# Kernel optimization log

Hardware: AMD Instinct MI355X
Metric: run time of the kernel (lower is better)

The kernel has to match this reference:

```python
import jax, jax.numpy as jnp
import numpy as np

H, B, T, DH = 16, 2, 2048, 64
MODEL_DIM = 1024


def setup_inputs() -> dict:
    key = jax.random.key(0)
    ks = jax.random.split(key, 5)
    q = jax.random.normal(ks[0], (H, B, T, DH), dtype=jnp.float32)
    k = jax.random.normal(ks[1], (H, B, T, DH), dtype=jnp.float32)
    v = jax.random.normal(ks[2], (H, B, T, DH), dtype=jnp.float32)
    Wo_w = jax.random.normal(ks[3], (MODEL_DIM, H * DH), dtype=jnp.float32) * 0.02
    Wo_b = jax.random.normal(ks[4], (MODEL_DIM,), dtype=jnp.float32) * 0.02
    return {"q": q, "k": k, "v": v, "Wo_w": Wo_w, "Wo_b": Wo_b}


def reference(q, k, v, Wo_w, Wo_b):
    # per-head scaled dot-product attention; scale uses per-head dk (=DH)
    scale = jnp.sqrt(jnp.asarray(DH, dtype=q.dtype))
    # scores: [H, B, T, T]
    scores = jnp.einsum('hbtd,hbsd->hbts', q, k) / scale
    # causal mask (additive -1e12 on strict upper triangle, matching torch code)
    mask = jnp.triu(jnp.ones((T, T), dtype=bool), 1)
    scores = scores + (-1e12) * mask.astype(scores.dtype)
    weights = jax.nn.softmax(scores, axis=-1)
    # context per head: [H, B, T, DH]
    context = jnp.einsum('hbts,hbsd->hbtd', weights, v)
    # concat heads along feature dim: [B, T, H*DH]
    context = jnp.transpose(context, (1, 2, 0, 3)).reshape(B, T, H * DH)
    # output projection (torch Linear: x @ W.T + b)
    return context @ Wo_w.T + Wo_b
```

## Files before the change

kernel.cpp:

```cpp
#include <hip/hip_runtime.h>

typedef __attribute__((ext_vector_type(8))) short bf16x8;
typedef __attribute__((ext_vector_type(4))) float f32x4;
typedef __attribute__((ext_vector_type(4))) unsigned int u32x4;
typedef __attribute__((ext_vector_type(4))) unsigned short u16x4;

#define H_ 16
#define B_ 2
#define T_ 2048
#define DH_ 64
#define MD_ 1024

static __device__ inline unsigned short f2bf(float f) {
    union { float f; unsigned u; } x; x.f = f;
    unsigned r = (x.u + 0x7fffu + ((x.u >> 16) & 1u)) >> 16;
    return (unsigned short)r;
}
static __device__ inline unsigned int pack_bf2(float lo, float hi) {
    return __builtin_amdgcn_perm(__float_as_uint(hi), __float_as_uint(lo), 0x07060302u);
}
static __device__ inline unsigned short hi16(float f) {
    return (unsigned short)(__float_as_uint(f) >> 16);
}

__global__ void cvt_k(const float* __restrict__ w, unsigned short* __restrict__ o, int n) {
    int i = (blockIdx.x * blockDim.x + threadIdx.x) * 4;
    if (i < n) {
        f32x4 x = *(const f32x4*)(w + i);
        u16x4 y;
        y[0] = f2bf(x[0]); y[1] = f2bf(x[1]); y[2] = f2bf(x[2]); y[3] = f2bf(x[3]);
        *(u16x4*)(o + i) = y;
    }
}

__global__ __launch_bounds__(256) void attn_k(const float* __restrict__ q,
                                              const float* __restrict__ k,
                                              const float* __restrict__ v,
                                              unsigned short* __restrict__ ctx) {
    const int flat = blockIdx.x;
    const int xcd = flat & 7, idx = flat >> 3;
    const int hb = xcd * 4 + (idx & 3);
    const int pair = idx >> 2;
    const int h = hb >> 1, b = hb & 1;
    const int tid = threadIdx.x;
    const int wave = tid >> 6, lane = tid & 63;
    const int ln = lane & 15, quad = lane >> 4;

    __shared__ __attribute__((aligned(16))) unsigned short kt[64][72];
    __shared__ __attribute__((aligned(16))) unsigned short vt[64][72];
    __shared__ __attribute__((aligned(16))) unsigned short pl[4][16][72];

    const long base = (long)hb * (T_ * DH_);
    const int krow = tid >> 2, kc = (tid & 3) * 16;
    const int vkp = tid & 31, vdg = tid >> 5;

    bf16x8 ones;
#pragma unroll
    for (int i = 0; i < 8; i++) ones[i] = (short)0x3F80;

#pragma unroll 1
    for (int halfsel = 0; halfsel < 2; halfsel++) {
        const int t = halfsel ? (31 - pair) : pair;
        const int nsteps = t + 1;
        const int q0w = t * 64 + wave * 16;

        bf16x8 qf0, qf1;
        {
            const float* qp = q + base + (long)(q0w + ln) * DH_ + quad * 8;
            f32x4 a0 = *(const f32x4*)qp;
            f32x4 a1 = *(const f32x4*)(qp + 4);
            f32x4 b0 = *(const f32x4*)(qp + 32);
            f32x4 b1 = *(const f32x4*)(qp + 36);
#pragma unroll
            for (int j = 0; j < 4; j++) {
                qf0[j]   = (short)f2bf(a0[j] * 0.125f);
                qf0[4+j] = (short)f2bf(a1[j] * 0.125f);
                qf1[j]   = (short)f2bf(b0[j] * 0.125f);
                qf1[4+j] = (short)f2bf(b1[j] * 0.125f);
            }
        }

        f32x4 oacc[4];
#pragma unroll
        for (int i = 0; i < 4; i++) oacc[i] = f32x4{0.f, 0.f, 0.f, 0.f};
        f32x4 lacc = f32x4{0.f, 0.f, 0.f, 0.f};

        f32x4 kr[4], va[2], vb[2];
        {
            const float* kp_ = k + base + (long)krow * DH_ + kc;
#pragma unroll
            for (int i = 0; i < 4; i++) kr[i] = *(const f32x4*)(kp_ + i * 4);
            const float* vp_ = v + base + (long)(2 * vkp) * DH_ + vdg * 8;
            va[0] = *(const f32x4*)vp_;       va[1] = *(const f32x4*)(vp_ + 4);
            vb[0] = *(const f32x4*)(vp_ + DH_); vb[1] = *(const f32x4*)(vp_ + DH_ + 4);
        }

#pragma unroll 1
        for (int step = 0; step < nsteps; step++) {
            __syncthreads();
            {
                u32x4 w0, w1;
                w0[0] = pack_bf2(kr[0][0], kr[0][1]); w0[1] = pack_bf2(kr[0][2], kr[0][3]);
                w0[2] = pack_bf2(kr[1][0], kr[1][1]); w0[3] = pack_bf2(kr[1][2], kr[1][3]);
                w1[0] = pack_bf2(kr[2][0], kr[2][1]); w1[1] = pack_bf2(kr[2][2], kr[2][3]);
                w1[2] = pack_bf2(kr[3][0], kr[3][1]); w1[3] = pack_bf2(kr[3][2], kr[3][3]);
                *(u32x4*)&kt[krow][kc]     = w0;
                *(u32x4*)&kt[krow][kc + 8] = w1;
#pragma unroll
                for (int j = 0; j < 4; j++)
                    ((unsigned int*)&vt[vdg * 8 + j][0])[vkp]     = pack_bf2(va[0][j], vb[0][j]);
#pragma unroll
                for (int j = 0; j < 4; j++)
                    ((unsigned int*)&vt[vdg * 8 + 4 + j][0])[vkp] = pack_bf2(va[1][j], vb[1][j]);
            }
            __syncthreads();

            if (step + 1 < nsteps) {
                const float* kp_ = k + base + (long)((step + 1) * 64 + krow) * DH_ + kc;
#pragma unroll
                for (int i = 0; i < 4; i++) kr[i] = *(const f32x4*)(kp_ + i * 4);
                const float* vp_ = v + base + (long)((step + 1) * 64 + 2 * vkp) * DH_ + vdg * 8;
                va[0] = *(const f32x4*)vp_;         va[1] = *(const f32x4*)(vp_ + 4);
                vb[0] = *(const f32x4*)(vp_ + DH_); vb[1] = *(const f32x4*)(vp_ + DH_ + 4);
            }

            f32x4 sa[4];
#pragma unroll
            for (int nt = 0; nt < 4; nt++) {
                bf16x8 kf0 = *(const bf16x8*)&kt[nt * 16 + ln][quad * 8];
                bf16x8 kf1 = *(const bf16x8*)&kt[nt * 16 + ln][32 + quad * 8];
                f32x4 a = f32x4{0.f, 0.f, 0.f, 0.f};
                a = __builtin_amdgcn_mfma_f32_16x16x32_bf16(qf0, kf0, a, 0, 0, 0);
                a = __builtin_amdgcn_mfma_f32_16x16x32_bf16(qf1, kf1, a, 0, 0, 0);
                sa[nt] = a;
            }

            if (step == nsteps - 1) {
                const int lr = wave * 16 + quad * 4;
#pragma unroll
                for (int nt = 0; nt < 4; nt++)
#pragma unroll
                    for (int r = 0; r < 4; r++) {
                        float p = __expf(sa[nt][r]);
                        if (nt * 16 + ln > lr + r) p = 0.f;
                        pl[wave][quad * 4 + r][nt * 16 + ln] = hi16(p);
                    }
            } else {
#pragma unroll
                for (int nt = 0; nt < 4; nt++)
#pragma unroll
                    for (int r = 0; r < 4; r++)
                        pl[wave][quad * 4 + r][nt * 16 + ln] = hi16(__expf(sa[nt][r]));
            }

            bf16x8 pf0 = *(const bf16x8*)&pl[wave][ln][quad * 8];
            bf16x8 pf1 = *(const bf16x8*)&pl[wave][ln][32 + quad * 8];

            lacc = __builtin_amdgcn_mfma_f32_16x16x32_bf16(pf0, ones, lacc, 0, 0, 0);
            lacc = __builtin_amdgcn_mfma_f32_16x16x32_bf16(pf1, ones, lacc, 0, 0, 0);

#pragma unroll
            for (int dt = 0; dt < 4; dt++) {
                bf16x8 vf0 = *(const bf16x8*)&vt[dt * 16 + ln][quad * 8];
                bf16x8 vf1 = *(const bf16x8*)&vt[dt * 16 + ln][32 + quad * 8];
                oacc[dt] = __builtin_amdgcn_mfma_f32_16x16x32_bf16(pf0, vf0, oacc[dt], 0, 0, 0);
                oacc[dt] = __builtin_amdgcn_mfma_f32_16x16x32_bf16(pf1, vf1, oacc[dt], 0, 0, 0);
            }
        }

#pragma unroll
        for (int r = 0; r < 4; r++) {
            float rl = __builtin_amdgcn_rcpf(lacc[r]);
            int row_g = q0w + quad * 4 + r;
#pragma unroll
            for (int dt = 0; dt < 4; dt++)
                ctx[(long)(b * T_ + row_g) * MD_ + h * 64 + dt * 16 + ln] =
                    f2bf(oacc[dt][r] * rl);
        }
    }
}

__global__ __launch_bounds__(256) void proj_k(const unsigned short* __restrict__ A,
                                              const unsigned short* __restrict__ Bw,
                                              const float* __restrict__ bias,
                                              float* __restrict__ out) {
    const int flat = blockIdx.x;
    const int xcd = flat & 7, idx = flat >> 3;
    const int n0 = (xcd * 2 + (idx & 1)) * 64;
    const int m0 = (idx >> 1) * 128;
    const int tid = threadIdx.x;
    const int wave = tid >> 6, lane = tid & 63;
    const int wm = wave >> 1, wn = wave & 1;
    const int ln = lane & 15, quad = lane >> 4;

    __shared__ __attribute__((aligned(16))) unsigned short As[128][72];
    __shared__ __attribute__((aligned(16))) unsigned short Bs[64][72];

    const int arow = tid >> 1, ac = (tid & 1) * 32;
    const int brow = tid >> 2, bc = (tid & 3) * 16;

    f32x4 acc[4][2];
#pragma unroll
    for (int i = 0; i < 4; i++)
#pragma unroll
        for (int j = 0; j < 2; j++) acc[i][j] = f32x4{0.f, 0.f, 0.f, 0.f};

    u32x4 ar[4], br[2];
    {
        const unsigned short* ap = A + (long)(m0 + arow) * 1024 + ac;
#pragma unroll
        for (int i = 0; i < 4; i++) ar[i] = *(const u32x4*)(ap + i * 8);
        const unsigned short* bp = Bw + (long)(n0 + brow) * 1024 + bc;
        br[0] = *(const u32x4*)bp; br[1] = *(const u32x4*)(bp + 8);
    }

#pragma unroll 1
    for (int ks = 0; ks < 1024; ks += 64) {
        __syncthreads();
#pragma unroll
        for (int i = 0; i < 4; i++) *(u32x4*)&As[arow][ac + i * 8] = ar[i];
        *(u32x4*)&Bs[brow][bc] = br[0];
        *(u32x4*)&Bs[brow][bc + 8] = br[1];
        __syncthreads();

        if (ks + 64 < 1024) {
            const unsigned short* ap = A + (long)(m0 + arow) * 1024 + ks + 64 + ac;
#pragma unroll
            for (int i = 0; i < 4; i++) ar[i] = *(const u32x4*)(ap + i * 8);
            const unsigned short* bp = Bw + (long)(n0 + brow) * 1024 + ks + 64 + bc;
            br[0] = *(const u32x4*)bp; br[1] = *(const u32x4*)(bp + 8);
        }

        bf16x8 af[4][2], bfr[2][2];
#pragma unroll
        for (int mt = 0; mt < 4; mt++) {
            af[mt][0] = *(const bf16x8*)&As[wm * 64 + mt * 16 + ln][quad * 8];
            af[mt][1] = *(const bf16x8*)&As[wm * 64 + mt * 16 + ln][32 + quad * 8];
        }
#pragma unroll
        for (int nt = 0; nt < 2; nt++) {
            bfr[nt][0] = *(const bf16x8*)&Bs[wn * 32 + nt * 16 + ln][quad * 8];
            bfr[nt][1] = *(const bf16x8*)&Bs[wn * 32 + nt * 16 + ln][32 + quad * 8];
        }
#pragma unroll
        for (int mt = 0; mt < 4; mt++)
#pragma unroll
            for (int nt = 0; nt < 2; nt++) {
                acc[mt][nt] = __builtin_amdgcn_mfma_f32_16x16x32_bf16(af[mt][0], bfr[nt][0], acc[mt][nt], 0, 0, 0);
                acc[mt][nt] = __builtin_amdgcn_mfma_f32_16x16x32_bf16(af[mt][1], bfr[nt][1], acc[mt][nt], 0, 0, 0);
            }
    }

#pragma unroll
    for (int nt = 0; nt < 2; nt++) {
        int col = n0 + wn * 32 + nt * 16 + ln;
        float bz = bias[col];
#pragma unroll
        for (int mt = 0; mt < 4; mt++)
#pragma unroll
            for (int r = 0; r < 4; r++) {
                int row = m0 + wm * 64 + mt * 16 + quad * 4 + r;
                out[(long)row * 1024 + col] = acc[mt][nt][r] + bz;
            }
    }
}

extern "C" void kernel_launch(void* const* d_in, const int* in_sizes, int n_in,
                              void* d_out, int out_size, void* d_ws, size_t ws_size,
                              hipStream_t stream) {
    const float* q    = (const float*)d_in[0];
    const float* k    = (const float*)d_in[1];
    const float* v    = (const float*)d_in[2];
    const float* Wo_w = (const float*)d_in[3];
    const float* Wo_b = (const float*)d_in[4];
    float* out = (float*)d_out;

    unsigned short* ctx = (unsigned short*)d_ws;
    unsigned short* wob = ctx + (size_t)4096 * 1024;

    cvt_k<<<1024, 256, 0, stream>>>(Wo_w, wob, MD_ * MD_);
    attn_k<<<512, 256, 0, stream>>>(q, k, v, ctx);
    proj_k<<<512, 256, 0, stream>>>(ctx, wob, Wo_b, out);
}
```

Measured before the change: 159.5 us.

## Pre-convert K and transposed V to bf16, split attention and projection grids

A new prep kernel converts K to bf16 and V to a transposed bf16 layout once, alongside the weight conversion. The attention kernel can then copy K and V tiles straight into LDS without packing or strided writes. Previously every query tile re-converted the same K and V from fp32. The attention grid now runs one query tile per block with 1024 blocks instead of pairing two tiles per block. The projection kernel uses 64x64 tiles, doubling its block count for more parallelism. In exchange it adds an extra global write and read of K and V and an extra prep pass.

Measured after the change: 153.5 us. 3.7% less time.

```diff
diff --git a/kernel.cpp b/kernel.cpp
--- a/kernel.cpp
+++ b/kernel.cpp
@@ -23,24 +23,71 @@
     return (unsigned short)(__float_as_uint(f) >> 16);
 }
 
-__global__ void cvt_k(const float* __restrict__ w, unsigned short* __restrict__ o, int n) {
-    int i = (blockIdx.x * blockDim.x + threadIdx.x) * 4;
-    if (i < n) {
+__global__ __launch_bounds__(256) void prep_k(const float* __restrict__ k,
+                                              const float* __restrict__ v,
+                                              const float* __restrict__ w,
+                                              unsigned short* __restrict__ kb,
+                                              unsigned short* __restrict__ vtb,
+                                              unsigned short* __restrict__ wob) {
+    __shared__ __attribute__((aligned(16))) unsigned short vt64[64][64];
+    const int blk = blockIdx.x;
+    const int tid = threadIdx.x;
+    if (blk < 1024) {
+        int i = (blk * 256 + tid) * 4;
         f32x4 x = *(const f32x4*)(w + i);
         u16x4 y;
         y[0] = f2bf(x[0]); y[1] = f2bf(x[1]); y[2] = f2bf(x[2]); y[3] = f2bf(x[3]);
-        *(u16x4*)(o + i) = y;
-    }
-}
-
-__global__ __launch_bounds__(256) void attn_k(const float* __restrict__ q,
-                                              const float* __restrict__ k,
-                                              const float* __restrict__ v,
-                                              unsigned short* __restrict__ ctx) {
-    const int flat = blockIdx.x;
-    const int xcd = flat & 7, idx = flat >> 3;
-    const int hb = xcd * 4 + (idx & 3);
-    const int pair = idx >> 2;
+        *(u16x4*)(wob + i) = y;
+    } else if (blk < 2048) {
+        int j = blk - 1024;
+        const int hb = j >> 5, s0 = (j & 31) * 64;
+        const int row = tid >> 2, c = (tid & 3) * 16;
+        const long off = (long)hb * (T_ * DH_) + (long)(s0 + row) * DH_ + c;
+        const float* p = k + off;
+        f32x4 a0 = *(const f32x4*)p;
+        f32x4 a1 = *(const f32x4*)(p + 4);
+        f32x4 a2 = *(const f32x4*)(p + 8);
+        f32x4 a3 = *(const f32x4*)(p + 12);
+        u32x4 w0, w1;
+        w0[0] = pack_bf2(a0[0], a0[1]); w0[1] = pack_bf2(a0[2], a0[3]);
+        w0[2] = pack_bf2(a1[0], a1[1]); w0[3] = pack_bf2(a1[2], a1[3]);
+        w1[0] = pack_bf2(a2[0], a2[1]); w1[1] = pack_bf2(a2[2], a2[3]);
+        w1[2] = pack_bf2(a3[0], a3[1]); w1[3] = pack_bf2(a3[2], a3[3]);
+        *(u32x4*)(kb + off) = w0;
+        *(u32x4*)(kb + off + 8) = w1;
+    } else {
+        int j = blk - 2048;
+        const int hb = j >> 5, s0 = (j & 31) * 64;
+        const int vkp = tid & 31, vdg = tid >> 5;
+        const float* vp = v + (long)hb * (T_ * DH_) + (long)(s0 + 2 * vkp) * DH_ + vdg * 8;
+        f32x4 va0 = *(const f32x4*)vp;
+        f32x4 va1 = *(const f32x4*)(vp + 4);
+        f32x4 vb0 = *(const f32x4*)(vp + DH_);
+        f32x4 vb1 = *(const f32x4*)(vp + DH_ + 4);
+#pragma unroll
+        for (int jj = 0; jj < 4; jj++) {
+            ((unsigned int*)&vt64[vdg * 8 + jj][0])[vkp]     = pack_bf2(va0[jj], vb0[jj]);
+            ((unsigned int*)&vt64[vdg * 8 + 4 + jj][0])[vkp] = pack_bf2(va1[jj], vb1[jj]);
+        }
+        __syncthreads();
+        const int dh = tid >> 2, kc = (tid & 3) * 16;
+        u32x4 o0 = *(const u32x4*)&vt64[dh][kc];
+        u32x4 o1 = *(const u32x4*)&vt64[dh][kc + 8];
+        unsigned short* op = vtb + (long)hb * (DH_ * T_) + (long)dh * T_ + s0 + kc;
+        *(u32x4*)op = o0;
+        *(u32x4*)(op + 8) = o1;
+    }
+}
+
+__global__ __launch_bounds__(256, 4) void attn_k(const float* __restrict__ q,
+                                                 const unsigned short* __restrict__ kb,
+                                                 const unsigned short* __restrict__ vtb,
+                                                 unsigned short* __restrict__ ctx) {
+    const int i = blockIdx.x;
+    const int xcd = i & 7, j = i >> 3;
+    const int cu = j & 31, l = j >> 5;
+    const int hb = xcd * 4 + l;
+    const int t = (l & 1) ? (31 - cu) : cu;
     const int h = hb >> 1, b = hb & 1;
     const int tid = threadIdx.x;
     const int wave = tid >> 6, lane = tid & 63;
@@ -50,219 +97,179 @@
     __shared__ __attribute__((aligned(16))) unsigned short vt[64][72];
     __shared__ __attribute__((aligned(16))) unsigned short pl[4][16][72];
 
-    const long base = (long)hb * (T_ * DH_);
-    const int krow = tid >> 2, kc = (tid & 3) * 16;
-    const int vkp = tid & 31, vdg = tid >> 5;
+    const long kbase = (long)hb * (T_ * DH_);
+    const long vbase = (long)hb * (DH_ * T_);
+    const int nsteps = t + 1;
+    const int q0w = t * 64 + wave * 16;
+    const int srow = tid >> 2, sc = (tid & 3) * 16;
 
     bf16x8 ones;
 #pragma unroll
-    for (int i = 0; i < 8; i++) ones[i] = (short)0x3F80;
+    for (int z = 0; z < 8; z++) ones[z] = (short)0x3F80;
+
+    bf16x8 qf0, qf1;
+    {
+        const float* qp = q + kbase + (long)(q0w + ln) * DH_ + quad * 8;
+        f32x4 a0 = *(const f32x4*)qp;
+        f32x4 a1 = *(const f32x4*)(qp + 4);
+        f32x4 b0 = *(const f32x4*)(qp + 32);
+        f32x4 b1 = *(const f32x4*)(qp + 36);
+#pragma unroll
+        for (int z = 0; z < 4; z++) {
+            qf0[z]   = (short)f2bf(a0[z] * 0.125f);
+            qf0[4+z] = (short)f2bf(a1[z] * 0.125f);
+            qf1[z]   = (short)f2bf(b0[z] * 0.125f);
+            qf1[4+z] = (short)f2bf(b1[z] * 0.125f);
+        }
+    }
+
+    f32x4 oacc[4];
+#pragma unroll
+    for (int z = 0; z < 4; z++) oacc[z] = f32x4{0.f, 0.f, 0.f, 0.f};
+    f32x4 lacc = f32x4{0.f, 0.f, 0.f, 0.f};
+
+    u32x4 kr0, kr1, vr0, vr1;
+    {
+        const unsigned short* kp = kb + kbase + (long)srow * DH_ + sc;
+        kr0 = *(const u32x4*)kp; kr1 = *(const u32x4*)(kp + 8);
+        const unsigned short* vp = vtb + vbase + (long)srow * T_ + sc;
+        vr0 = *(const u32x4*)vp; vr1 = *(const u32x4*)(vp + 8);
+    }
 
 #pragma unroll 1
-    for (int halfsel = 0; halfsel < 2; halfsel++) {
-        const int t = halfsel ? (31 - pair) : pair;
-        const int nsteps = t + 1;
-        const int q0w = t * 64 + wave * 16;
-
-        bf16x8 qf0, qf1;
-        {
-            const float* qp = q + base + (long)(q0w + ln) * DH_ + quad * 8;
-            f32x4 a0 = *(const f32x4*)qp;
-            f32x4 a1 = *(const f32x4*)(qp + 4);
-            f32x4 b0 = *(const f32x4*)(qp + 32);
-            f32x4 b1 = *(const f32x4*)(qp + 36);
-#pragma unroll
-            for (int j = 0; j < 4; j++) {
-                qf0[j]   = (short)f2bf(a0[j] * 0.125f);
-                qf0[4+j] = (short)f2bf(a1[j] * 0.125f);
-                qf1[j]   = (short)f2bf(b0[j] * 0.125f);
-                qf1[4+j] = (short)f2bf(b1[j] * 0.125f);
-            }
-        }
-
-        f32x4 oacc[4];
-#pragma unroll
-        for (int i = 0; i < 4; i++) oacc[i] = f32x4{0.f, 0.f, 0.f, 0.f};
-        f32x4 lacc = f32x4{0.f, 0.f, 0.f, 0.f};
-
-        f32x4 kr[4], va[2], vb[2];
-        {
-            const float* kp_ = k + base + (long)krow * DH_ + kc;
-#pragma unroll
-            for (int i = 0; i < 4; i++) kr[i] = *(const f32x4*)(kp_ + i * 4);
-            const float* vp_ = v + base + (long)(2 * vkp) * DH_ + vdg * 8;
-            va[0] = *(const f32x4*)vp_;       va[1] = *(const f32x4*)(vp_ + 4);
-            vb[0] = *(const f32x4*)(vp_ + DH_); vb[1] = *(const f32x4*)(vp_ + DH_ + 4);
-        }
-
-#pragma unroll 1
-        for (int step = 0; step < nsteps; step++) {
-            __syncthreads();
-            {
-                u32x4 w0, w1;
-                w0[0] = pack_bf2(kr[0][0], kr[0][1]); w0[1] = pack_bf2(kr[0][2], kr[0][3]);
-                w0[2] = pack_bf2(kr[1][0], kr[1][1]); w0[3] = pack_bf2(kr[1][2], kr[1][3]);
-                w1[0] = pack_bf2(kr[2][0], kr[2][1]); w1[1] = pack_bf2(kr[2][2], kr[2][3]);
-                w1[2] = pack_bf2(kr[3][0], kr[3][1]); w1[3] = pack_bf2(kr[3][2], kr[3][3]);
-                *(u32x4*)&kt[krow][kc]     = w0;
-                *(u32x4*)&kt[krow][kc + 8] = w1;
-#pragma unroll
-                for (int j = 0; j < 4; j++)
-                    ((unsigned int*)&vt[vdg * 8 + j][0])[vkp]     = pack_bf2(va[0][j], vb[0][j]);
-#pragma unroll
-                for (int j = 0; j < 4; j++)
-                    ((unsigned int*)&vt[vdg * 8 + 4 + j][0])[vkp] = pack_bf2(va[1][j], vb[1][j]);
-            }
-            __syncthreads();
-
-            if (step + 1 < nsteps) {
-                const float* kp_ = k + base + (long)((step + 1) * 64 + krow) * DH_ + kc;
-#pragma unroll
-                for (int i = 0; i < 4; i++) kr[i] = *(const f32x4*)(kp_ + i * 4);
-                const float* vp_ = v + base + (long)((step + 1) * 64 + 2 * vkp) * DH_ + vdg * 8;
-                va[0] = *(const f32x4*)vp_;         va[1] = *(const f32x4*)(vp_ + 4);
-                vb[0] = *(const f32x4*)(vp_ + DH_); vb[1] = *(const f32x4*)(vp_ + DH_ + 4);
-            }
-
-            f32x4 sa[4];
-#pragma unroll
-            for (int nt = 0; nt < 4; nt++) {
-                bf16x8 kf0 = *(const bf16x8*)&kt[nt * 16 + ln][quad * 8];
-                bf16x8 kf1 = *(const bf16x8*)&kt[nt * 16 + ln][32 + quad * 8];
-                f32x4 a = f32x4{0.f, 0.f, 0.f, 0.f};
-                a = __builtin_amdgcn_mfma_f32_16x16x32_bf16(qf0, kf0, a, 0, 0, 0);
-                a = __builtin_amdgcn_mfma_f32_16x16x32_bf16(qf1, kf1, a, 0, 0, 0);
-                sa[nt] = a;
-            }
-
-            if (step == nsteps - 1) {
-                const int lr = wave * 16 + quad * 4;
-#pragma unroll
-                for (int nt = 0; nt < 4; nt++)
-#pragma unroll
-                    for (int r = 0; r < 4; r++) {
-                        float p = __expf(sa[nt][r]);
-                        if (nt * 16 + ln > lr + r) p = 0.f;
-                        pl[wave][quad * 4 + r][nt * 16 + ln] = hi16(p);
-                    }
-            } else {
-#pragma unroll
-                for (int nt = 0; nt < 4; nt++)
-#pragma unroll
-                    for (int r = 0; r < 4; r++)
-                        pl[wave][quad * 4 + r][nt * 16 + ln] = hi16(__expf(sa[nt][r]));
-            }
-
-            bf16x8 pf0 = *(const bf16x8*)&pl[wave][ln][quad * 8];
-            bf16x8 pf1 = *(const bf16x8*)&pl[wave][ln][32 + quad * 8];
-
-            lacc = __builtin_amdgcn_mfma_f32_16x16x32_bf16(pf0, ones, lacc, 0, 0, 0);
-            lacc = __builtin_amdgcn_mfma_f32_16x16x32_bf16(pf1, ones, lacc, 0, 0, 0);
-
-#pragma unroll
-            for (int dt = 0; dt < 4; dt++) {
-                bf16x8 vf0 = *(const bf16x8*)&vt[dt * 16 + ln][quad * 8];
-                bf16x8 vf1 = *(const bf16x8*)&vt[dt * 16 + ln][32 + quad * 8];
-                oacc[dt] = __builtin_amdgcn_mfma_f32_16x16x32_bf16(pf0, vf0, oacc[dt], 0, 0, 0);
-                oacc[dt] = __builtin_amdgcn_mfma_f32_16x16x32_bf16(pf1, vf1, oacc[dt], 0, 0, 0);
-            }
-        }
-
-#pragma unroll
-        for (int r = 0; r < 4; r++) {
-            float rl = __builtin_amdgcn_rcpf(lacc[r]);
-            int row_g = q0w + quad * 4 + r;
-#pragma unroll
-            for (int dt = 0; dt < 4; dt++)
-                ctx[(long)(b * T_ + row_g) * MD_ + h * 64 + dt * 16 + ln] =
-                    f2bf(oacc[dt][r] * rl);
-        }
-    }
-}
-
-__global__ __launch_bounds__(256) void proj_k(const unsigned short* __restrict__ A,
-                                              const unsigned short* __restrict__ Bw,
-                                              const float* __restrict__ bias,
-                                              float* __restrict__ out) {
-    const int flat = blockIdx.x;
-    const int xcd = flat & 7, idx = flat >> 3;
-    const int n0 = (xcd * 2 + (idx & 1)) * 64;
-    const int m0 = (idx >> 1) * 128;
+    for (int step = 0; step < nsteps; step++) {
+        __syncthreads();
+        *(u32x4*)&kt[srow][sc]     = kr0;
+        *(u32x4*)&kt[srow][sc + 8] = kr1;
+        *(u32x4*)&vt[srow][sc]     = vr0;
+        *(u32x4*)&vt[srow][sc + 8] = vr1;
+        __syncthreads();
+
+        if (step + 1 < nsteps) {
+            const unsigned short* kp = kb + kbase + (long)((step + 1) * 64 + srow) * DH_ + sc;
+            kr0 = *(const u32x4*)kp; kr1 = *(const u32x4*)(kp + 8);
+            const unsigned short* vp = vtb + vbase + (long)srow * T_ + (step + 1) * 64 + sc;
+            vr0 = *(const u32x4*)vp; vr1 = *(const u32x4*)(vp + 8);
+        }
+
+        f32x4 sa[4];
+#pragma unroll
+        for (int nt = 0; nt < 4; nt++) {
+            bf16x8 kf0 = *(const bf16x8*)&kt[nt * 16 + ln][quad * 8];
+            bf16x8 kf1 = *(const bf16x8*)&kt[nt * 16 + ln][32 + quad * 8];
+            f32x4 a = f32x4{0.f, 0.f, 0.f, 0.f};
+            a = __builtin_amdgcn_mfma_f32_16x16x32_bf16(qf0, kf0, a, 0, 0, 0);
+            a = __builtin_amdgcn_mfma_f32_16x16x32_bf16(qf1, kf1, a, 0, 0, 0);
+            sa[nt] = a;
+        }
+
+        if (step == nsteps - 1) {
+            const int lr = wave * 16 + quad * 4;
+#pragma unroll
+            for (int nt = 0; nt < 4; nt++)
+#pragma unroll
+                for (int r = 0; r < 4; r++) {
+                    float p = __expf(sa[nt][r]);
+                    if (nt * 16 + ln > lr + r) p = 0.f;
+                    pl[wave][quad * 4 + r][nt * 16 + ln] = hi16(p);
+                }
+        } else {
+#pragma unroll
+            for (int nt = 0; nt < 4; nt++)
+#pragma unroll
+                for (int r = 0; r < 4; r++)
+                    pl[wave][quad * 4 + r][nt * 16 + ln] = hi16(__expf(sa[nt][r]));
+        }
+
+        bf16x8 pf0 = *(const bf16x8*)&pl[wave][ln][quad * 8];
+        bf16x8 pf1 = *(const bf16x8*)&pl[wave][ln][32 + quad * 8];
+
+#pragma unroll
+        for (int dt = 0; dt < 4; dt++) {
+            bf16x8 vf0 = *(const bf16x8*)&vt[dt * 16 + ln][quad * 8];
+            bf16x8 vf1 = *(const bf16x8*)&vt[dt * 16 + ln][32 + quad * 8];
+            oacc[dt] = __builtin_amdgcn_mfma_f32_16x16x32_bf16(pf0, vf0, oacc[dt], 0, 0, 0);
+            oacc[dt] = __builtin_amdgcn_mfma_f32_16x16x32_bf16(pf1, vf1, oacc[dt], 0, 0, 0);
+        }
+        lacc = __builtin_amdgcn_mfma_f32_16x16x32_bf16(pf0, ones, lacc, 0, 0, 0);
+        lacc = __builtin_amdgcn_mfma_f32_16x16x32_bf16(pf1, ones, lacc, 0, 0, 0);
+    }
+
+#pragma unroll
+    for (int r = 0; r < 4; r++) {
+        float rl = __builtin_amdgcn_rcpf(lacc[r]);
+        int row_g = q0w + quad * 4 + r;
+#pragma unroll
+        for (int dt = 0; dt < 4; dt++)
+            ctx[(long)(b * T_ + row_g) * MD_ + h * 64 + dt * 16 + ln] =
+                f2bf(oacc[dt][r] * rl);
+    }
+}
+
+__global__ __launch_bounds__(256, 4) void proj_k(const unsigned short* __restrict__ A,
+                                                 const unsigned short* __restrict__ Bw,
+                                                 const float* __restrict__ bias,
+                                                 float* __restrict__ out) {
+    const int i = blockIdx.x;
+    const int n0 = ((i & 7) * 2 + ((i >> 3) & 1)) * 64;
+    const int m0 = (i >> 4) * 64;
     const int tid = threadIdx.x;
     const int wave = tid >> 6, lane = tid & 63;
-    const int wm = wave >> 1, wn = wave & 1;
     const int ln = lane & 15, quad = lane >> 4;
 
-    __shared__ __attribute__((aligned(16))) unsigned short As[128][72];
+    __shared__ __attribute__((aligned(16))) unsigned short As[64][72];
     __shared__ __attribute__((aligned(16))) unsigned short Bs[64][72];
 
-    const int arow = tid >> 1, ac = (tid & 1) * 32;
-    const int brow = tid >> 2, bc = (tid & 3) * 16;
-
-    f32x4 acc[4][2];
-#pragma unroll
-    for (int i = 0; i < 4; i++)
-#pragma unroll
-        for (int j = 0; j < 2; j++) acc[i][j] = f32x4{0.f, 0.f, 0.f, 0.f};
-
-    u32x4 ar[4], br[2];
+    const int srow = tid >> 2, sc = (tid & 3) * 16;
+
+    f32x4 acc[4];
+#pragma unroll
+    for (int z = 0; z < 4; z++) acc[z] = f32x4{0.f, 0.f, 0.f, 0.f};
+
+    u32x4 ar0, ar1, br0, br1;
     {
-        const unsigned short* ap = A + (long)(m0 + arow) * 1024 + ac;
-#pragma unroll
-        for (int i = 0; i < 4; i++) ar[i] = *(const u32x4*)(ap + i * 8);
-        const unsigned short* bp = Bw + (long)(n0 + brow) * 1024 + bc;
-        br[0] = *(const u32x4*)bp; br[1] = *(const u32x4*)(bp + 8);
+        const unsigned short* ap = A + (long)(m0 + srow) * 1024 + sc;
+        ar0 = *(const u32x4*)ap; ar1 = *(const u32x4*)(ap + 8);
+        const unsigned short* bp = Bw + (long)(n0 + srow) * 1024 + sc;
+        br0 = *(const u32x4*)bp; br1 = *(const u32x4*)(bp + 8);
     }
 
 #pragma unroll 1
     for (int ks = 0; ks < 1024; ks += 64) {
         __syncthreads();
-#pragma unroll
-        for (int i = 0; i < 4; i++) *(u32x4*)&As[arow][ac + i * 8] = ar[i];
-        *(u32x4*)&Bs[brow][bc] = br[0];
-        *(u32x4*)&Bs[brow][bc + 8] = br[1];
+        *(u32x4*)&As[srow][sc]     = ar0;
+        *(u32x4*)&As[srow][sc + 8] = ar1;
+        *(u32x4*)&Bs[srow][sc]     = br0;
+        *(u32x4*)&Bs[srow][sc + 8] = br1;
         __syncthreads();
 
         if (ks + 64 < 1024) {
-            const unsigned short* ap = A + (long)(m0 + arow) * 1024 + ks + 64 + ac;
-#pragma unroll
-            for (int i = 0; i < 4; i++) ar[i] = *(const u32x4*)(ap + i * 8);
-            const unsigned short* bp = Bw + (long)(n0 + brow) * 1024 + ks + 64 + bc;
-            br[0] = *(const u32x4*)bp; br[1] = *(const u32x4*)(bp + 8);
-        }
-
-        bf16x8 af[4][2], bfr[2][2];
+            const unsigned short* ap = A + (long)(m0 + srow) * 1024 + ks + 64 + sc;
+            ar0 = *(const u32x4*)ap; ar1 = *(const u32x4*)(ap + 8);
+            const unsigned short* bp = Bw + (long)(n0 + srow) * 1024 + ks + 64 + sc;
+            br0 = *(const u32x4*)bp; br1 = *(const u32x4*)(bp + 8);
+        }
+
+        bf16x8 bf0 = *(const bf16x8*)&Bs[wave * 16 + ln][quad * 8];
+        bf16x8 bf1 = *(const bf16x8*)&Bs[wave * 16 + ln][32 + quad * 8];
 #pragma unroll
         for (int mt = 0; mt < 4; mt++) {
-            af[mt][0] = *(const bf16x8*)&As[wm * 64 + mt * 16 + ln][quad * 8];
-            af[mt][1] = *(const bf16x8*)&As[wm * 64 + mt * 16 + ln][32 + quad * 8];
-        }
-#pragma unroll
-        for (int nt = 0; nt < 2; nt++) {
-            bfr[nt][0] = *(const bf16x8*)&Bs[wn * 32 + nt * 16 + ln][quad * 8];
-            bfr[nt][1] = *(const bf16x8*)&Bs[wn * 32 + nt * 16 + ln][32 + quad * 8];
-        }
-#pragma unroll
-        for (int mt = 0; mt < 4; mt++)
-#pragma unroll
-            for (int nt = 0; nt < 2; nt++) {
-                acc[mt][nt] = __builtin_amdgcn_mfma_f32_16x16x32_bf16(af[mt][0], bfr[nt][0], acc[mt][nt], 0, 0, 0);
-                acc[mt][nt] = __builtin_amdgcn_mfma_f32_16x16x32_bf16(af[mt][1], bfr[nt][1], acc[mt][nt], 0, 0, 0);
-            }
-    }
-
-#pragma unroll
-    for (int nt = 0; nt < 2; nt++) {
-        int col = n0 + wn * 32 + nt * 16 + ln;
-        float bz = bias[col];
-#pragma unroll
-        for (int mt = 0; mt < 4; mt++)
-#pragma unroll
-            for (int r = 0; r < 4; r++) {
-                int row = m0 + wm * 64 + mt * 16 + quad * 4 + r;
-                out[(long)row * 1024 + col] = acc[mt][nt][r] + bz;
-            }
-    }
+            bf16x8 af0 = *(const bf16x8*)&As[mt * 16 + ln][quad * 8];
+            bf16x8 af1 = *(const bf16x8*)&As[mt * 16 + ln][32 + quad * 8];
+            acc[mt] = __builtin_amdgcn_mfma_f32_16x16x32_bf16(af0, bf0, acc[mt], 0, 0, 0);
+            acc[mt] = __builtin_amdgcn_mfma_f32_16x16x32_bf16(af1, bf1, acc[mt], 0, 0, 0);
+        }
+    }
+
+    int col = n0 + wave * 16 + ln;
+    float bz = bias[col];
+#pragma unroll
+    for (int mt = 0; mt < 4; mt++)
+#pragma unroll
+        for (int r = 0; r < 4; r++) {
+            int row = m0 + mt * 16 + quad * 4 + r;
+            out[(long)row * 1024 + col] = acc[mt][r] + bz;
+        }
 }
 
 extern "C" void kernel_launch(void* const* d_in, const int* in_sizes, int n_in,
@@ -277,8 +284,10 @@
 
     unsigned short* ctx = (unsigned short*)d_ws;
     unsigned short* wob = ctx + (size_t)4096 * 1024;
-
-    cvt_k<<<1024, 256, 0, stream>>>(Wo_w, wob, MD_ * MD_);
-    attn_k<<<512, 256, 0, stream>>>(q, k, v, ctx);
-    proj_k<<<512, 256, 0, stream>>>(ctx, wob, Wo_b, out);
-}
+    unsigned short* kbb = wob + (size_t)1024 * 1024;
+    unsigned short* vtb = kbb + (size_t)32 * 2048 * 64;
+
+    prep_k<<<3072, 256, 0, stream>>>(k, v, Wo_w, kbb, vtb, wob);
+    attn_k<<<1024, 256, 0, stream>>>(q, kbb, vtb, ctx);
+    proj_k<<<1024, 256, 0, stream>>>(ctx, wob, Wo_b, out);
+}
```
